# Kernel tuning notes

Measured on AMD Instinct MI355X. Metric: run time of the kernel, lower is better.

The kernel has to match this reference:

```python
import jax, jax.numpy as jnp
import numpy as np

TOPK = 20

def setup_inputs() -> dict:
    key = jax.random.key(0)
    k1, k2, k3 = jax.random.split(key, 3)
    B, n, D = 4, 4096, 256
    src1 = jax.random.normal(k1, (B, n, D), dtype=jnp.float32)
    src2 = jax.random.normal(k2, (B, n, D), dtype=jnp.float32)
    memoryMartix = jax.random.normal(k3, (n, n), dtype=jnp.float32)
    return {"src1": src1, "src2": src2, "memoryMartix": memoryMartix}

def reference(src1, src2, memoryMartix):
    # softmax over dim=1 of the [n, n] memory matrix
    probs = jax.nn.softmax(memoryMartix, axis=1)            # [n, n]
    # top-k along dim=1: values and indices per row
    vtopk, ind = jax.lax.top_k(probs, TOPK)                 # [n, k], [n, k]
    # gather src2 rows per output position: [B, n, k, D]
    gathered = jnp.take(src2, ind, axis=1)
    # weighted sum over the k selected neighbors
    src = jnp.einsum('bnkd,nk->bnd', gathered, vtopk)       # [B, n, D]
    return src + src1
```

## Files before the change

kernel.cpp:

```cpp
#include <hip/hip_runtime.h>
#include <math.h>

#define TOPK  20
#define NROW  4096
#define DDIM  256
#define NB    4
#define NCHUNK 16

#define AWPB   2
#define ABLOCK (AWPB * 64)
#define BBLOCK 256

typedef float vf4 __attribute__((ext_vector_type(4)));

__device__ __forceinline__ void wave_lds_fence() {
    asm volatile("s_waitcnt lgkmcnt(0)" ::: "memory");
}

__device__ __forceinline__ bool lex_gt(float av, int ai, float bv, int bi) {
    return (av > bv) || (av == bv && ai < bi);
}

__device__ __forceinline__ void bitonic64_desc(float& v, int& i, int lane) {
#pragma unroll
    for (int k = 2; k <= 64; k <<= 1) {
#pragma unroll
        for (int j = k >> 1; j > 0; j >>= 1) {
            float pv = __shfl_xor(v, j, 64);
            int   pi = __shfl_xor(i, j, 64);
            bool takeBig = ((lane & k) == 0) == ((lane & j) == 0);
            bool pBig = lex_gt(pv, pi, v, i);
            if (takeBig == pBig) { v = pv; i = pi; }
        }
    }
}

__global__ __launch_bounds__(ABLOCK, 4) void topk_select(
    const float* __restrict__ mem,
    float* __restrict__ ws_w,
    int*   __restrict__ ws_i)
{
    __shared__ float cand_v[AWPB][64];
    __shared__ int   cand_i[AWPB][64];
    const int wave = threadIdx.x >> 6;
    const int lane = threadIdx.x & 63;
    const int n    = blockIdx.x * AWPB + wave;

    const float4* mrow = (const float4*)(mem + (size_t)n * NROW);
    float4 v4[NCHUNK];
#pragma unroll
    for (int j = 0; j < NCHUNK; ++j) v4[j] = mrow[lane + 64 * j];

    float bv = -INFINITY; int bi = 0x7fffffff;
#pragma unroll
    for (int j = 0; j < NCHUNK; ++j) {
        const int base = 4 * lane + 256 * j;
        if (v4[j].x > bv) { bv = v4[j].x; bi = base + 0; }
        if (v4[j].y > bv) { bv = v4[j].y; bi = base + 1; }
        if (v4[j].z > bv) { bv = v4[j].z; bi = base + 2; }
        if (v4[j].w > bv) { bv = v4[j].w; bi = base + 3; }
    }

    float sv = bv; int si = bi;
    bitonic64_desc(sv, si, lane);
    const float rowmax = __shfl(sv, 0, 64);
    const float tv     = __shfl(sv, 19, 64);
    const int   ti     = __shfl(si, 19, 64);

    float lsum = 0.f;
#pragma unroll
    for (int j = 0; j < NCHUNK; ++j) {
        lsum += __expf(v4[j].x - rowmax) + __expf(v4[j].y - rowmax)
              + __expf(v4[j].z - rowmax) + __expf(v4[j].w - rowmax);
    }
#pragma unroll
    for (int o = 32; o > 0; o >>= 1) lsum += __shfl_xor(lsum, o, 64);
    const float inv_denom = 1.0f / lsum;

    int cnt = 0;
#pragma unroll
    for (int j = 0; j < NCHUNK; ++j) {
        const int base = 4 * lane + 256 * j;
        cnt += (v4[j].x > tv) || (v4[j].x == tv && (base + 0) <= ti);
        cnt += (v4[j].y > tv) || (v4[j].y == tv && (base + 1) <= ti);
        cnt += (v4[j].z > tv) || (v4[j].z == tv && (base + 2) <= ti);
        cnt += (v4[j].w > tv) || (v4[j].w == tv && (base + 3) <= ti);
    }
    int incl = cnt;
#pragma unroll
    for (int o = 1; o < 64; o <<= 1) {
        int t = __shfl_up(incl, o, 64);
        if (lane >= o) incl += t;
    }
    const int total = __builtin_amdgcn_readfirstlane(__shfl(incl, 63, 64));

    float* gw = ws_w + (size_t)n * TOPK;
    int*   gi = ws_i + (size_t)n * TOPK;

    if (total <= 64) {
        int off = incl - cnt;
#pragma unroll
        for (int j = 0; j < NCHUNK; ++j) {
            const int base = 4 * lane + 256 * j;
            const float4 q = v4[j];
            if ((q.x > tv) || (q.x == tv && (base + 0) <= ti)) { cand_v[wave][off] = q.x; cand_i[wave][off] = base + 0; ++off; }
            if ((q.y > tv) || (q.y == tv && (base + 1) <= ti)) { cand_v[wave][off] = q.y; cand_i[wave][off] = base + 1; ++off; }
            if ((q.z > tv) || (q.z == tv && (base + 2) <= ti)) { cand_v[wave][off] = q.z; cand_i[wave][off] = base + 2; ++off; }
            if ((q.w > tv) || (q.w == tv && (base + 3) <= ti)) { cand_v[wave][off] = q.w; cand_i[wave][off] = base + 3; ++off; }
        }
        wave_lds_fence();
        float cv = -INFINITY; int ci = 0x7fffffff;
        if (lane < total) { cv = cand_v[wave][lane]; ci = cand_i[wave][lane]; }
        bitonic64_desc(cv, ci, lane);
        if (lane < TOPK) {
            gw[lane] = __expf(cv - rowmax) * inv_denom;
            gi[lane] = ci;
        }
    } else {
        unsigned long long dead = 0;
        float cv = bv; int ci = bi;
        for (int r = 0; r < TOPK; ++r) {
            float wv = cv; int wi = ci;
#pragma unroll
            for (int o = 32; o > 0; o >>= 1) {
                float ov = __shfl_xor(wv, o, 64);
                int   oi = __shfl_xor(wi, o, 64);
                if (lex_gt(ov, oi, wv, wi)) { wv = ov; wi = oi; }
            }
            if (lane == 0) {
                gw[r] = __expf(wv - rowmax) * inv_denom;
                gi[r] = wi;
            }
            if (ci == wi) {
                const int e = 4 * ((wi >> 8) & 15) + (wi & 3);
                dead |= (1ull << e);
                cv = -INFINITY; ci = 0x7fffffff;
#pragma unroll
                for (int j = 0; j < NCHUNK; ++j) {
                    const int base = 4 * lane + 256 * j;
                    if (!((dead >> (4 * j + 0)) & 1) && v4[j].x > cv) { cv = v4[j].x; ci = base + 0; }
                    if (!((dead >> (4 * j + 1)) & 1) && v4[j].y > cv) { cv = v4[j].y; ci = base + 1; }
                    if (!((dead >> (4 * j + 2)) & 1) && v4[j].z > cv) { cv = v4[j].z; ci = base + 2; }
                    if (!((dead >> (4 * j + 3)) & 1) && v4[j].w > cv) { cv = v4[j].w; ci = base + 3; }
                }
            }
        }
    }
}

__global__ __launch_bounds__(BBLOCK, 4) void gather_epilogue(
    const float* __restrict__ src1,
    const float* __restrict__ src2,
    const float* __restrict__ ws_w,
    const int*   __restrict__ ws_i,
    float* __restrict__ out)
{
    const int bid  = blockIdx.x;
    const int xcd  = bid & 7;
    const int b    = xcd >> 1;
    const int h    = xcd & 1;
    const int grp  = bid >> 3;
    const int wave = threadIdx.x >> 6;
    const int lane = threadIdx.x & 63;
    const int half = lane >> 5;
    const int dl   = lane & 31;
    const int n    = grp * 8 + wave * 2 + half;
    const int d4   = h * 32 + dl;

    const float* gw = ws_w + (size_t)n * TOPK;
    const int*   gi = ws_i + (size_t)n * TOPK;
    float wk[TOPK]; int ik[TOPK];
#pragma unroll
    for (int k = 0; k < TOPK; ++k) { wk[k] = gw[k]; ik[k] = gi[k]; }

    const vf4* s2b = (const vf4*)src2 + (size_t)b * NROW * (DDIM / 4);
    const size_t rowbase = ((size_t)b * NROW + n) * (DDIM / 4) + d4;

    vf4 acc = __builtin_nontemporal_load((const vf4*)src1 + rowbase);
#pragma unroll
    for (int k = 0; k < TOPK; ++k) {
        const vf4 g = s2b[(size_t)ik[k] * (DDIM / 4) + d4];
        acc += wk[k] * g;
    }
    __builtin_nontemporal_store(acc, (vf4*)out + rowbase);
}

extern "C" void kernel_launch(void* const* d_in, const int* in_sizes, int n_in,
                              void* d_out, int out_size, void* d_ws, size_t ws_size,
                              hipStream_t stream) {
    const float* src1 = (const float*)d_in[0];
    const float* src2 = (const float*)d_in[1];
    const float* mem  = (const float*)d_in[2];
    float* out = (float*)d_out;

    float* ws_w = (float*)d_ws;
    int*   ws_i = (int*)d_ws + (size_t)NROW * TOPK;

    topk_select<<<NROW / AWPB, ABLOCK, 0, stream>>>(mem, ws_w, ws_i);
    gather_epilogue<<<NROW, BBLOCK, 0, stream>>>(src1, src2, ws_w, ws_i, out);
}
```

Measured before the change: 151.1 us.

## Stage rows in LDS, fuse softmax sum without max, use atomic candidate compaction

The top-k kernel now streams each row into LDS instead of holding 64 floats per lane in registers. It computes the row max and the exp-sum in one pass by skipping the max subtraction. Candidate compaction moves from a wave prefix scan to LDS atomics. The aim is lower register pressure, higher occupancy and one less pass over the data. In exchange it relies on exp not overflowing for the input range, adds LDS traffic and atomic contention, and candidate order is no longer deterministic (the bitonic sort afterwards fixes this).

```diff
diff --git a/kernel.cpp b/kernel.cpp
--- a/kernel.cpp
+++ b/kernel.cpp
@@ -35,85 +35,69 @@
     }
 }
 
-__global__ __launch_bounds__(ABLOCK, 4) void topk_select(
+__global__ __launch_bounds__(ABLOCK) void topk_select(
     const float* __restrict__ mem,
     float* __restrict__ ws_w,
     int*   __restrict__ ws_i)
 {
+    __shared__ vf4   rowbuf[AWPB][NROW / 4];
     __shared__ float cand_v[AWPB][64];
     __shared__ int   cand_i[AWPB][64];
+    __shared__ int   ccnt[AWPB];
+
     const int wave = threadIdx.x >> 6;
     const int lane = threadIdx.x & 63;
     const int n    = blockIdx.x * AWPB + wave;
 
-    const float4* mrow = (const float4*)(mem + (size_t)n * NROW);
-    float4 v4[NCHUNK];
-#pragma unroll
-    for (int j = 0; j < NCHUNK; ++j) v4[j] = mrow[lane + 64 * j];
+    if (lane == 0) ccnt[wave] = 0;
+
+    const vf4* mrow = (const vf4*)(mem + (size_t)n * NROW);
 
     float bv = -INFINITY; int bi = 0x7fffffff;
-#pragma unroll
-    for (int j = 0; j < NCHUNK; ++j) {
-        const int base = 4 * lane + 256 * j;
-        if (v4[j].x > bv) { bv = v4[j].x; bi = base + 0; }
-        if (v4[j].y > bv) { bv = v4[j].y; bi = base + 1; }
-        if (v4[j].z > bv) { bv = v4[j].z; bi = base + 2; }
-        if (v4[j].w > bv) { bv = v4[j].w; bi = base + 3; }
-    }
-
-    float sv = bv; int si = bi;
-    bitonic64_desc(sv, si, lane);
-    const float rowmax = __shfl(sv, 0, 64);
-    const float tv     = __shfl(sv, 19, 64);
-    const int   ti     = __shfl(si, 19, 64);
-
     float lsum = 0.f;
 #pragma unroll
     for (int j = 0; j < NCHUNK; ++j) {
-        lsum += __expf(v4[j].x - rowmax) + __expf(v4[j].y - rowmax)
-              + __expf(v4[j].z - rowmax) + __expf(v4[j].w - rowmax);
+        const vf4 q = mrow[lane + 64 * j];
+        rowbuf[wave][64 * j + lane] = q;
+        const int base = 4 * lane + 256 * j;
+        if (q.x > bv) { bv = q.x; bi = base + 0; }
+        if (q.y > bv) { bv = q.y; bi = base + 1; }
+        if (q.z > bv) { bv = q.z; bi = base + 2; }
+        if (q.w > bv) { bv = q.w; bi = base + 3; }
+        lsum += __expf(q.x) + __expf(q.y) + __expf(q.z) + __expf(q.w);
     }
 #pragma unroll
     for (int o = 32; o > 0; o >>= 1) lsum += __shfl_xor(lsum, o, 64);
     const float inv_denom = 1.0f / lsum;
 
-    int cnt = 0;
+    float sv = bv; int si = bi;
+    bitonic64_desc(sv, si, lane);
+    const float tv = __shfl(sv, 19, 64);
+    const int   ti = __shfl(si, 19, 64);
+
+    wave_lds_fence();
+
 #pragma unroll
     for (int j = 0; j < NCHUNK; ++j) {
+        const vf4 q = rowbuf[wave][64 * j + lane];
         const int base = 4 * lane + 256 * j;
-        cnt += (v4[j].x > tv) || (v4[j].x == tv && (base + 0) <= ti);
-        cnt += (v4[j].y > tv) || (v4[j].y == tv && (base + 1) <= ti);
-        cnt += (v4[j].z > tv) || (v4[j].z == tv && (base + 2) <= ti);
-        cnt += (v4[j].w > tv) || (v4[j].w == tv && (base + 3) <= ti);
+        if ((q.x > tv) || (q.x == tv && (base + 0) <= ti)) { int s = atomicAdd(&ccnt[wave], 1); if (s < 64) { cand_v[wave][s] = q.x; cand_i[wave][s] = base + 0; } }
+        if ((q.y > tv) || (q.y == tv && (base + 1) <= ti)) { int s = atomicAdd(&ccnt[wave], 1); if (s < 64) { cand_v[wave][s] = q.y; cand_i[wave][s] = base + 1; } }
+        if ((q.z > tv) || (q.z == tv && (base + 2) <= ti)) { int s = atomicAdd(&ccnt[wave], 1); if (s < 64) { cand_v[wave][s] = q.z; cand_i[wave][s] = base + 2; } }
+        if ((q.w > tv) || (q.w == tv && (base + 3) <= ti)) { int s = atomicAdd(&ccnt[wave], 1); if (s < 64) { cand_v[wave][s] = q.w; cand_i[wave][s] = base + 3; } }
     }
-    int incl = cnt;
-#pragma unroll
-    for (int o = 1; o < 64; o <<= 1) {
-        int t = __shfl_up(incl, o, 64);
-        if (lane >= o) incl += t;
-    }
-    const int total = __builtin_amdgcn_readfirstlane(__shfl(incl, 63, 64));
+    wave_lds_fence();
+    const int total = ccnt[wave];
 
     float* gw = ws_w + (size_t)n * TOPK;
     int*   gi = ws_i + (size_t)n * TOPK;
 
     if (total <= 64) {
-        int off = incl - cnt;
-#pragma unroll
-        for (int j = 0; j < NCHUNK; ++j) {
-            const int base = 4 * lane + 256 * j;
-            const float4 q = v4[j];
-            if ((q.x > tv) || (q.x == tv && (base + 0) <= ti)) { cand_v[wave][off] = q.x; cand_i[wave][off] = base + 0; ++off; }
-            if ((q.y > tv) || (q.y == tv && (base + 1) <= ti)) { cand_v[wave][off] = q.y; cand_i[wave][off] = base + 1; ++off; }
-            if ((q.z > tv) || (q.z == tv && (base + 2) <= ti)) { cand_v[wave][off] = q.z; cand_i[wave][off] = base + 2; ++off; }
-            if ((q.w > tv) || (q.w == tv && (base + 3) <= ti)) { cand_v[wave][off] = q.w; cand_i[wave][off] = base + 3; ++off; }
-        }
-        wave_lds_fence();
         float cv = -INFINITY; int ci = 0x7fffffff;
         if (lane < total) { cv = cand_v[wave][lane]; ci = cand_i[wave][lane]; }
         bitonic64_desc(cv, ci, lane);
         if (lane < TOPK) {
-            gw[lane] = __expf(cv - rowmax) * inv_denom;
+            gw[lane] = __expf(cv) * inv_denom;
             gi[lane] = ci;
         }
     } else {
@@ -128,7 +112,7 @@
                 if (lex_gt(ov, oi, wv, wi)) { wv = ov; wi = oi; }
             }
             if (lane == 0) {
-                gw[r] = __expf(wv - rowmax) * inv_denom;
+                gw[r] = __expf(wv) * inv_denom;
                 gi[r] = wi;
             }
             if (ci == wi) {
@@ -137,11 +121,12 @@
                 cv = -INFINITY; ci = 0x7fffffff;
 #pragma unroll
                 for (int j = 0; j < NCHUNK; ++j) {
+                    const vf4 q = rowbuf[wave][64 * j + lane];
                     const int base = 4 * lane + 256 * j;
-                    if (!((dead >> (4 * j + 0)) & 1) && v4[j].x > cv) { cv = v4[j].x; ci = base + 0; }
-                    if (!((dead >> (4 * j + 1)) & 1) && v4[j].y > cv) { cv = v4[j].y; ci = base + 1; }
-                    if (!((dead >> (4 * j + 2)) & 1) && v4[j].z > cv) { cv = v4[j].z; ci = base + 2; }
-                    if (!((dead >> (4 * j + 3)) & 1) && v4[j].w > cv) { cv = v4[j].w; ci = base + 3; }
+                    if (!((dead >> (4 * j + 0)) & 1) && q.x > cv) { cv = q.x; ci = base + 0; }
+                    if (!((dead >> (4 * j + 1)) & 1) && q.y > cv) { cv = q.y; ci = base + 1; }
+                    if (!((dead >> (4 * j + 2)) & 1) && q.z > cv) { cv = q.z; ci = base + 2; }
+                    if (!((dead >> (4 * j + 3)) & 1) && q.w > cv) { cv = q.w; ci = base + 3; }
                 }
             }
         }
```

Result: slower. 161.7 us (+7.1%).
